# Kernel tuning notes

Hardware: AMD Instinct MI355X
Metric: run time of the kernel (lower is better)

The kernel has to match this reference:

```python
import jax, jax.numpy as jnp
import numpy as np

N_NODES = 50000
N_EDGES = 1600000
D_IN = 128
D_OUT = 32
N_HEADS = 4


def setup_inputs() -> dict:
    key = jax.random.key(0)
    k1, k2, k3, k4 = jax.random.split(key, 4)
    x = jax.random.normal(k1, (N_NODES, D_IN), dtype=jnp.float32)
    edge_index = jax.random.randint(k2, (2, N_EDGES), 0, N_NODES, dtype=jnp.int64)
    W = jax.random.normal(k3, (N_HEADS, D_IN, D_OUT), dtype=jnp.float32) * 0.01
    a = jax.random.normal(k4, (N_HEADS, 2 * D_OUT), dtype=jnp.float32) * 0.01
    return {"x": x, "edge_index": edge_index, "W": W, "a": a}


def reference(x, edge_index, W, a):
    N = x.shape[0]
    K, d_in, d_out = W.shape
    # Per-head projected node features: [N, K, d_out]
    Wh = jnp.einsum('ni,kio->nko', x, W)
    src, tgt = edge_index[0], edge_index[1]
    # cat([Wh[src], Wh[tgt]]) . a  ==  Wh[src].a[:, :d] + Wh[tgt].a[:, d:]
    s_src = jnp.einsum('nkd,kd->nk', Wh, a[:, :d_out])  # [N, K]
    s_tgt = jnp.einsum('nkd,kd->nk', Wh, a[:, d_out:])  # [N, K]
    e = s_src[src] + s_tgt[tgt]                          # [E, K]
    e = jnp.where(e > 0, e, 0.2 * e)                     # LeakyReLU(0.2)
    # Segment-softmax over incoming edges of each target node
    e_max = jax.ops.segment_max(e, tgt, num_segments=N)  # [N, K], -inf for empty
    e_max = jnp.where(jnp.isfinite(e_max), e_max, 0.0)
    e_exp = jnp.exp(e - e_max[tgt])                      # [E, K]
    e_sum = jax.ops.segment_sum(e_exp, tgt, num_segments=N)  # [N, K]
    alpha = e_exp / (e_sum[tgt] + 1e-10)                 # [E, K]
    # Weighted scatter-add aggregation: [N, K, d_out]
    weighted = alpha[:, :, None] * Wh[src]
    out = jax.ops.segment_sum(weighted, tgt, num_segments=N)
    out = out.reshape(N, K * d_out)
    return jnp.where(out > 0, out, jnp.expm1(out))       # ELU
```

## Files before the change

kernel.cpp:

```cpp
#include <hip/hip_runtime.h>
#include <math.h>

#define N_HEADS 4
#define D_IN    128
#define D_OUT   32
#define D_TOT   128
#define TN      64
#define XPAD    132
#define BSH     6
#define BNODES  64
#define MAXNB   1024
#define EPT     16
#define CAP     2560

static __device__ __forceinline__ unsigned short f2bf(float f) {
    unsigned u = __float_as_uint(f);
    u += 0x7fffu + ((u >> 16) & 1u);
    return (unsigned short)(u >> 16);
}

__global__ __launch_bounds__(256) void front_kernel(
    const float* __restrict__ x,
    const float* __restrict__ W,
    const float* __restrict__ a,
    const int*  __restrict__ ei,
    int*  __restrict__ cursor,
    unsigned int* __restrict__ bbuf,
    unsigned int* __restrict__ Whu,
    float* __restrict__ s_src,
    float* __restrict__ s_tgt,
    int N, int E, int nProj, int nb) {

    __shared__ float xs[TN][XPAD];
    const int t = threadIdx.x;

    if (blockIdx.x >= nProj) {
        int* cnt = (int*)xs;
        for (int i = t; i < nb; i += 256) cnt[i] = 0;
        __syncthreads();

        const int e0 = (blockIdx.x - nProj) * (256 * EPT);
        int src[EPT], tgt[EPT];
        #pragma unroll
        for (int i = 0; i < EPT; ++i) {
            int e = e0 + i * 256 + t;
            if (e < E) {
                src[i] = ei[e];
                tgt[i] = ei[E + e];
                atomicAdd(&cnt[tgt[i] >> BSH], 1);
            } else {
                src[i] = -1; tgt[i] = 0;
            }
        }
        __syncthreads();
        for (int b = t; b < nb; b += 256)
            if (cnt[b]) cnt[b] = atomicAdd(&cursor[b], cnt[b]);
        __syncthreads();
        #pragma unroll
        for (int i = 0; i < EPT; ++i) {
            if (src[i] >= 0) {
                int b = tgt[i] >> BSH;
                int pos = atomicAdd(&cnt[b], 1);
                if (pos < CAP)
                    bbuf[(size_t)b * CAP + pos] =
                        ((unsigned)(tgt[i] & (BNODES - 1)) << 16) | (unsigned)src[i];
            }
        }
        return;
    }

    const int n0 = blockIdx.x * TN;
    {
        const int r  = t >> 2;
        const int c0 = (t & 3) * 32;
        int nn = n0 + r; if (nn >= N) nn = N - 1;
        const float4* src = (const float4*)(x + (size_t)nn * D_IN + c0);
        #pragma unroll
        for (int j = 0; j < 8; ++j)
            *(float4*)&xs[r][c0 + j * 4] = src[j];
    }
    __syncthreads();

    const int fg = t & 15;
    const int ng = t >> 4;
    const int f0 = fg * 8;
    const int k  = f0 >> 5;
    const int o0 = f0 & 31;
    const float* Wf = W + k * (D_IN * D_OUT) + o0;

    float acc[4][8];
    #pragma unroll
    for (int nl = 0; nl < 4; ++nl)
        #pragma unroll
        for (int j = 0; j < 8; ++j) acc[nl][j] = 0.f;

    #pragma unroll 2
    for (int i = 0; i < D_IN; i += 4) {
        float4 wa[4], wb[4];
        #pragma unroll
        for (int ii = 0; ii < 4; ++ii) {
            wa[ii] = *(const float4*)(Wf + (i + ii) * D_OUT);
            wb[ii] = *(const float4*)(Wf + (i + ii) * D_OUT + 4);
        }
        #pragma unroll
        for (int nl = 0; nl < 4; ++nl) {
            const float4 xv = *(const float4*)&xs[ng * 4 + nl][i];
            const float xr[4] = {xv.x, xv.y, xv.z, xv.w};
            #pragma unroll
            for (int ii = 0; ii < 4; ++ii) {
                acc[nl][0] = fmaf(xr[ii], wa[ii].x, acc[nl][0]);
                acc[nl][1] = fmaf(xr[ii], wa[ii].y, acc[nl][1]);
                acc[nl][2] = fmaf(xr[ii], wa[ii].z, acc[nl][2]);
                acc[nl][3] = fmaf(xr[ii], wa[ii].w, acc[nl][3]);
                acc[nl][4] = fmaf(xr[ii], wb[ii].x, acc[nl][4]);
                acc[nl][5] = fmaf(xr[ii], wb[ii].y, acc[nl][5]);
                acc[nl][6] = fmaf(xr[ii], wb[ii].z, acc[nl][6]);
                acc[nl][7] = fmaf(xr[ii], wb[ii].w, acc[nl][7]);
            }
        }
    }

    const float4 as0 = *(const float4*)(a + k * (2 * D_OUT) + o0);
    const float4 as1 = *(const float4*)(a + k * (2 * D_OUT) + o0 + 4);
    const float4 at0 = *(const float4*)(a + k * (2 * D_OUT) + D_OUT + o0);
    const float4 at1 = *(const float4*)(a + k * (2 * D_OUT) + D_OUT + o0 + 4);

    #pragma unroll
    for (int nl = 0; nl < 4; ++nl) {
        const int n = n0 + ng * 4 + nl;
        if (n < N) {
            unsigned int p[4];
            #pragma unroll
            for (int j = 0; j < 4; ++j)
                p[j] = (unsigned)f2bf(acc[nl][2 * j]) |
                       ((unsigned)f2bf(acc[nl][2 * j + 1]) << 16);
            *(uint4*)&Whu[(size_t)n * 64 + fg * 4] = make_uint4(p[0], p[1], p[2], p[3]);

            float vs = acc[nl][0] * as0.x + acc[nl][1] * as0.y +
                       acc[nl][2] * as0.z + acc[nl][3] * as0.w +
                       acc[nl][4] * as1.x + acc[nl][5] * as1.y +
                       acc[nl][6] * as1.z + acc[nl][7] * as1.w;
            float vt = acc[nl][0] * at0.x + acc[nl][1] * at0.y +
                       acc[nl][2] * at0.z + acc[nl][3] * at0.w +
                       acc[nl][4] * at1.x + acc[nl][5] * at1.y +
                       acc[nl][6] * at1.z + acc[nl][7] * at1.w;
            vs += __shfl_xor(vs, 1, 64); vs += __shfl_xor(vs, 2, 64);
            vt += __shfl_xor(vt, 1, 64); vt += __shfl_xor(vt, 2, 64);
            if ((fg & 3) == 0) {
                s_src[n * N_HEADS + k] = vs;
                s_tgt[n * N_HEADS + k] = vt;
            }
        }
    }
}

__global__ __launch_bounds__(256) void finalize_kernel(
    const unsigned int* __restrict__ bbuf,
    const int* __restrict__ cursor,
    int* __restrict__ rs_beg,
    int* __restrict__ rs_end,
    unsigned short* __restrict__ rec,
    int N) {

    __shared__ int hist[BNODES];
    __shared__ int cur[BNODES];
    const int b = blockIdx.x;
    const int t = threadIdx.x;
    const int cnt = cursor[b];
    const int base = b * CAP;

    if (t < BNODES) hist[t] = 0;
    __syncthreads();
    for (int j = t; j < cnt; j += 256)
        atomicAdd(&hist[bbuf[base + j] >> 16], 1);
    __syncthreads();

    if (t < BNODES) {
        int v = hist[t];
        int vp = (v + 1) & ~1;
        int incl = vp;
        #pragma unroll
        for (int off = 1; off < 64; off <<= 1) {
            int tv = __shfl_up(incl, off, 64);
            if (t >= off) incl += tv;
        }
        int excl = incl - vp;
        if (excl > CAP) excl = CAP;
        int e2 = excl + v;
        if (e2 > CAP) e2 = CAP;
        cur[t] = excl;
        int n = b * BNODES + t;
        if (n < N) {
            rs_beg[n] = base + excl;
            rs_end[n] = base + e2;
        }
    }
    __syncthreads();

    for (int j = t; j < cnt; j += 256) {
        unsigned v = bbuf[base + j];
        int pos = atomicAdd(&cur[v >> 16], 1);
        if (pos < CAP)
            rec[base + pos] = (unsigned short)(v & 0xFFFFu);
    }
}

__global__ __launch_bounds__(256) void agg_kernel(
    const unsigned short* __restrict__ rec,
    const int* __restrict__ rs_beg,
    const int* __restrict__ rs_end,
    const float* __restrict__ s_src,
    const float* __restrict__ s_tgt,
    const unsigned int* __restrict__ Whu,
    float* __restrict__ out, int N) {

    const int n = blockIdx.x * 4 + (threadIdx.x >> 6);
    if (n >= N) return;
    const int t = threadIdx.x & 63;
    const int k = t >> 4;

    const int beg = rs_beg[n];
    const int end = rs_end[n];
    const float stk = s_tgt[((size_t)n << 2) + k];
    const unsigned* rec32 = (const unsigned*)rec;

    float den = 0.f, nx = 0.f, ny = 0.f;
    int j = beg;
    for (; j + 16 <= end; j += 16) {
        unsigned d[8];
        #pragma unroll
        for (int q = 0; q < 8; ++q) d[q] = rec32[(j >> 1) + q];
        int sv[16];
        #pragma unroll
        for (int q = 0; q < 8; ++q) {
            sv[2 * q]     = (int)(d[q] & 0xFFFFu);
            sv[2 * q + 1] = (int)(d[q] >> 16);
        }
        unsigned w[16];
        #pragma unroll
        for (int q = 0; q < 16; ++q)
            w[q] = Whu[((unsigned)sv[q] << 6) + (unsigned)t];
        float ss[16];
        #pragma unroll
        for (int q = 0; q < 16; ++q)
            ss[q] = s_src[((size_t)sv[q] << 2) + k];
        #pragma unroll
        for (int q = 0; q < 16; ++q) {
            float av = ss[q] + stk;
            av = fmaxf(av, 0.2f * av);
            const float ev = __expf(av);
            den += ev;
            nx = fmaf(ev, __uint_as_float(w[q] << 16), nx);
            ny = fmaf(ev, __uint_as_float(w[q] & 0xffff0000u), ny);
        }
    }
    if (j < end) {
        const int dmax = (((n >> 6) + 1) * CAP) >> 1;
        unsigned d[8];
        #pragma unroll
        for (int q = 0; q < 8; ++q) {
            int di = (j >> 1) + q;
            d[q] = rec32[di < dmax ? di : dmax - 1];
        }
        const int sv0 = (int)(d[0] & 0xFFFFu);
        #pragma unroll
        for (int q = 0; q < 16; ++q) {
            const bool ok = (j + q) < end;
            int sv = (q & 1) ? (int)(d[q >> 1] >> 16)
                             : (int)(d[q >> 1] & 0xFFFFu);
            sv = ok ? sv : sv0;
            const unsigned w = Whu[((unsigned)sv << 6) + (unsigned)t];
            const float ssv = s_src[((size_t)sv << 2) + k];
            float av = ssv + stk;
            av = fmaxf(av, 0.2f * av);
            const float ev = ok ? __expf(av) : 0.f;
            den += ev;
            nx = fmaf(ev, __uint_as_float(w << 16), nx);
            ny = fmaf(ev, __uint_as_float(w & 0xffff0000u), ny);
        }
    }

    const float inv = 1.f / (den + 1e-10f);
    float ox = nx * inv, oy = ny * inv;
    ox = ox > 0.f ? ox : expm1f(ox);
    oy = oy > 0.f ? oy : expm1f(oy);
    *(float2*)&out[((size_t)n << 7) + (t << 1)] = make_float2(ox, oy);
}

extern "C" void kernel_launch(void* const* d_in, const int* in_sizes, int n_in,
                              void* d_out, int out_size, void* d_ws, size_t ws_size,
                              hipStream_t stream) {
    const float* x  = (const float*)d_in[0];
    const int*   ei = (const int*)d_in[1];
    const float* W  = (const float*)d_in[2];
    const float* a  = (const float*)d_in[3];
    float* out = (float*)d_out;

    const int N = in_sizes[0] / D_IN;
    const int E = in_sizes[1] / 2;
    const int nb = (N + BNODES - 1) >> BSH;

    unsigned int* Whu = (unsigned int*)d_ws;
    float* s_src    = (float*)(Whu + (size_t)N * 64);
    float* s_tgt    = s_src + (size_t)N * N_HEADS;
    int*   cursor   = (int*)(s_tgt + (size_t)N * N_HEADS);
    int*   rs_beg   = cursor + nb;
    int*   rs_end   = rs_beg + N;
    unsigned int* bbuf = (unsigned int*)(rs_end + N);
    unsigned short* rec = (unsigned short*)(bbuf + (size_t)nb * CAP);

    hipMemsetAsync(cursor, 0, (size_t)nb * sizeof(int), stream);

    const int nProj = (N + TN - 1) / TN;
    const int nBkt  = (E + 256 * EPT - 1) / (256 * EPT);
    front_kernel<<<nProj + nBkt, 256, 0, stream>>>(
        x, W, a, ei, cursor, bbuf, Whu, s_src, s_tgt, N, E, nProj, nb);

    finalize_kernel<<<nb, 256, 0, stream>>>(bbuf, cursor, rs_beg, rs_end, rec, N);

    agg_kernel<<<(N + 3) / 4, 256, 0, stream>>>(
        rec, rs_beg, rs_end, s_src, s_tgt, Whu, out, N);
}
```

Baseline: 122.9 us.

## Compute edge exponentials once per lane and share via LDS in aggregation

Each lane of a 16-lane head group now computes the attention exponential for one edge and writes it to shared memory. All lanes then read the 16 weights back, instead of every lane redundantly loading s_src and evaluating exp for all 16 edges. The denominator comes from a shuffle reduction, and the separate tail path is replaced by masking. To make this safe, per-node record segments are padded to 8 entries so they can be read with aligned 16-byte loads, CAP is raised, and workspace buffers are 256-byte aligned. This adds LDS traffic and a larger padded footprint, and it relies on the wavefront executing in lockstep because no barrier guards the LDS exchange.

```diff
diff --git a/kernel.cpp b/kernel.cpp
--- a/kernel.cpp
+++ b/kernel.cpp
@@ -11,7 +11,7 @@
 #define BNODES  64
 #define MAXNB   1024
 #define EPT     16
-#define CAP     2560
+#define CAP     2816
 
 static __device__ __forceinline__ unsigned short f2bf(float f) {
     unsigned u = __float_as_uint(f);
@@ -177,7 +177,7 @@
 
     if (t < BNODES) {
         int v = hist[t];
-        int vp = (v + 1) & ~1;
+        int vp = (v + 7) & ~7;
         int incl = vp;
         #pragma unroll
         for (int off = 1; off < 64; off <<= 1) {
@@ -214,73 +214,66 @@
     const unsigned int* __restrict__ Whu,
     float* __restrict__ out, int N) {
 
-    const int n = blockIdx.x * 4 + (threadIdx.x >> 6);
+    __shared__ float evs[4][64];
+    const int wid = threadIdx.x >> 6;
+    const int n = blockIdx.x * 4 + wid;
     if (n >= N) return;
-    const int t = threadIdx.x & 63;
-    const int k = t >> 4;
+    const int t   = threadIdx.x & 63;
+    const int k   = t >> 4;
+    const int i16 = t & 15;
 
     const int beg = rs_beg[n];
     const int end = rs_end[n];
     const float stk = s_tgt[((size_t)n << 2) + k];
-    const unsigned* rec32 = (const unsigned*)rec;
-
-    float den = 0.f, nx = 0.f, ny = 0.f;
-    int j = beg;
-    for (; j + 16 <= end; j += 16) {
-        unsigned d[8];
-        #pragma unroll
-        for (int q = 0; q < 8; ++q) d[q] = rec32[(j >> 1) + q];
+    const uint4* rec128 = (const uint4*)rec;
+
+    float denp = 0.f, nx = 0.f, ny = 0.f;
+    for (int j = beg; j < end; j += 16) {
+        const uint4 da = rec128[(unsigned)(j >> 3)];
+        const uint4 db = rec128[(unsigned)(j >> 3) + 1];
+        const int own = j + i16;
+        const unsigned svo = rec[own];
+        const float ssv = s_src[((size_t)svo << 2) + k];
+        float av = ssv + stk;
+        av = fmaxf(av, 0.2f * av);
+        const float evv = (own < end) ? __expf(av) : 0.f;
+        denp += evv;
+        evs[wid][t] = evv;
+
         int sv[16];
-        #pragma unroll
-        for (int q = 0; q < 8; ++q) {
-            sv[2 * q]     = (int)(d[q] & 0xFFFFu);
-            sv[2 * q + 1] = (int)(d[q] >> 16);
-        }
+        sv[0]  = (int)(da.x & 0xffffu); sv[1]  = (int)(da.x >> 16);
+        sv[2]  = (int)(da.y & 0xffffu); sv[3]  = (int)(da.y >> 16);
+        sv[4]  = (int)(da.z & 0xffffu); sv[5]  = (int)(da.z >> 16);
+        sv[6]  = (int)(da.w & 0xffffu); sv[7]  = (int)(da.w >> 16);
+        sv[8]  = (int)(db.x & 0xffffu); sv[9]  = (int)(db.x >> 16);
+        sv[10] = (int)(db.y & 0xffffu); sv[11] = (int)(db.y >> 16);
+        sv[12] = (int)(db.z & 0xffffu); sv[13] = (int)(db.z >> 16);
+        sv[14] = (int)(db.w & 0xffffu); sv[15] = (int)(db.w >> 16);
+
         unsigned w[16];
         #pragma unroll
         for (int q = 0; q < 16; ++q)
             w[q] = Whu[((unsigned)sv[q] << 6) + (unsigned)t];
-        float ss[16];
-        #pragma unroll
-        for (int q = 0; q < 16; ++q)
-            ss[q] = s_src[((size_t)sv[q] << 2) + k];
+
+        float e[16];
+        *(float4*)&e[0]  = *(const float4*)&evs[wid][(k << 4) + 0];
+        *(float4*)&e[4]  = *(const float4*)&evs[wid][(k << 4) + 4];
+        *(float4*)&e[8]  = *(const float4*)&evs[wid][(k << 4) + 8];
+        *(float4*)&e[12] = *(const float4*)&evs[wid][(k << 4) + 12];
+
         #pragma unroll
         for (int q = 0; q < 16; ++q) {
-            float av = ss[q] + stk;
-            av = fmaxf(av, 0.2f * av);
-            const float ev = __expf(av);
-            den += ev;
-            nx = fmaf(ev, __uint_as_float(w[q] << 16), nx);
-            ny = fmaf(ev, __uint_as_float(w[q] & 0xffff0000u), ny);
-        }
-    }
-    if (j < end) {
-        const int dmax = (((n >> 6) + 1) * CAP) >> 1;
-        unsigned d[8];
-        #pragma unroll
-        for (int q = 0; q < 8; ++q) {
-            int di = (j >> 1) + q;
-            d[q] = rec32[di < dmax ? di : dmax - 1];
-        }
-        const int sv0 = (int)(d[0] & 0xFFFFu);
-        #pragma unroll
-        for (int q = 0; q < 16; ++q) {
-            const bool ok = (j + q) < end;
-            int sv = (q & 1) ? (int)(d[q >> 1] >> 16)
-                             : (int)(d[q >> 1] & 0xFFFFu);
-            sv = ok ? sv : sv0;
-            const unsigned w = Whu[((unsigned)sv << 6) + (unsigned)t];
-            const float ssv = s_src[((size_t)sv << 2) + k];
-            float av = ssv + stk;
-            av = fmaxf(av, 0.2f * av);
-            const float ev = ok ? __expf(av) : 0.f;
-            den += ev;
-            nx = fmaf(ev, __uint_as_float(w << 16), nx);
-            ny = fmaf(ev, __uint_as_float(w & 0xffff0000u), ny);
-        }
-    }
-
-    const float inv = 1.f / (den + 1e-10f);
+            nx = fmaf(e[q], __uint_as_float(w[q] << 16), nx);
+            ny = fmaf(e[q], __uint_as_float(w[q] & 0xffff0000u), ny);
+        }
+    }
+
+    denp += __shfl_xor(denp, 1, 64);
+    denp += __shfl_xor(denp, 2, 64);
+    denp += __shfl_xor(denp, 4, 64);
+    denp += __shfl_xor(denp, 8, 64);
+
+    const float inv = 1.f / (denp + 1e-10f);
     float ox = nx * inv, oy = ny * inv;
     ox = ox > 0.f ? ox : expm1f(ox);
     oy = oy > 0.f ? oy : expm1f(oy);
@@ -300,14 +293,16 @@
     const int E = in_sizes[1] / 2;
     const int nb = (N + BNODES - 1) >> BSH;
 
-    unsigned int* Whu = (unsigned int*)d_ws;
-    float* s_src    = (float*)(Whu + (size_t)N * 64);
-    float* s_tgt    = s_src + (size_t)N * N_HEADS;
-    int*   cursor   = (int*)(s_tgt + (size_t)N * N_HEADS);
-    int*   rs_beg   = cursor + nb;
-    int*   rs_end   = rs_beg + N;
-    unsigned int* bbuf = (unsigned int*)(rs_end + N);
-    unsigned short* rec = (unsigned short*)(bbuf + (size_t)nb * CAP);
+    char* p = (char*)d_ws;
+    auto align256 = [](size_t v) { return (v + 255) & ~(size_t)255; };
+    unsigned int* Whu = (unsigned int*)p;      p += align256((size_t)N * 64 * 4);
+    float* s_src    = (float*)p;               p += align256((size_t)N * N_HEADS * 4);
+    float* s_tgt    = (float*)p;               p += align256((size_t)N * N_HEADS * 4);
+    int*   cursor   = (int*)p;                 p += align256((size_t)nb * 4);
+    int*   rs_beg   = (int*)p;                 p += align256((size_t)N * 4);
+    int*   rs_end   = (int*)p;                 p += align256((size_t)N * 4);
+    unsigned int* bbuf = (unsigned int*)p;     p += align256((size_t)nb * CAP * 4);
+    unsigned short* rec = (unsigned short*)p;
 
     hipMemsetAsync(cursor, 0, (size_t)nb * sizeof(int), stream);
 
```

After: 122.7 us. Within noise of the previous version (-0.2%).
